# Kernel tuning notes

Measured on AMD Instinct MI355X. Metric: run time of the kernel, lower is better.

## Reference

```python
import jax, jax.numpy as jnp
import numpy as np

NUM_NODES = 50000
NODE_DIM = 32
EDGE_DIM = 7
HIDDEN_DIM = 64
NUM_EDGES = 200000


def setup_inputs() -> dict:
    key = jax.random.key(0)
    ks = jax.random.split(key, 12)
    s = lambda *d: 1.0 / np.sqrt(d[0])
    return {
        "edge_index": jax.random.randint(ks[0], (2, NUM_EDGES), 0, NUM_NODES, dtype=jnp.int64)
        if jax.config.jax_enable_x64 else jax.random.randint(ks[0], (2, NUM_EDGES), 0, NUM_NODES, dtype=jnp.int32),
        "edge_attr": jax.random.normal(ks[1], (NUM_EDGES, EDGE_DIM), dtype=jnp.float32),
        # learned parameters
        "node_emb": jax.random.normal(ks[2], (NUM_NODES, NODE_DIM), dtype=jnp.float32),
        "w_nn": jax.random.normal(ks[3], (EDGE_DIM, NODE_DIM * HIDDEN_DIM), dtype=jnp.float32) * s(EDGE_DIM),
        "b_nn": jnp.zeros((NODE_DIM * HIDDEN_DIM,), dtype=jnp.float32),
        "root_w": jax.random.normal(ks[4], (NODE_DIM, HIDDEN_DIM), dtype=jnp.float32) * s(NODE_DIM),
        "conv_bias": jnp.zeros((HIDDEN_DIM,), dtype=jnp.float32),
        "w_e1": jax.random.normal(ks[5], (2 * HIDDEN_DIM + EDGE_DIM, 64), dtype=jnp.float32) * s(2 * HIDDEN_DIM + EDGE_DIM),
        "b_e1": jnp.zeros((64,), dtype=jnp.float32),
        "w_e2": jax.random.normal(ks[6], (64, 2), dtype=jnp.float32) * s(64),
        "b_e2": jnp.zeros((2,), dtype=jnp.float32),
    }


def reference(edge_index, edge_attr, node_emb, w_nn, b_nn, root_w, conv_bias,
              w_e1, b_e1, w_e2, b_e2):
    src, dst = edge_index[0], edge_index[1]
    x = node_emb  # [N, node_dim]
    # NNConv: per-edge weight matrix from edge MLP (Linear + ReLU)
    w_edge = jax.nn.relu(edge_attr @ w_nn + b_nn).reshape(-1, NODE_DIM, HIDDEN_DIM)  # [E, in, out]
    # gather source features, per-edge matmul, scatter-add to dst (aggr='add')
    msg = jnp.einsum("ei,eio->eo", x[src], w_edge)  # [E, hidden]
    agg = jax.ops.segment_sum(msg, dst, num_segments=NUM_NODES)  # [N, hidden]
    h = jax.nn.relu(agg + x @ root_w + conv_bias)  # conv root term + bias, then outer ReLU
    # edge classifier MLP
    edge_repr = jnp.concatenate([h[src], h[dst], edge_attr], axis=1)  # [E, 2H+edge_dim]
    out = jax.nn.relu(edge_repr @ w_e1 + b_e1) @ w_e2 + b_e2  # [E, 2]
    return out
```

## Files before the change

### kernel.cpp

```cpp
#include <hip/hip_runtime.h>
#include <hip/hip_bf16.h>

#define NUM_NODES 50000
#define NODE_DIM 32
#define EDGE_DIM 7
#define HIDDEN_DIM 64
#define NUM_EDGES 200000

#define INIT_BLOCKS ((NUM_NODES + 127) / 128)
#define PREP_BLOCKS ((5 * 4 * 64 * 8 + 255) / 256)

typedef __attribute__((ext_vector_type(8))) short bf16x8;
typedef __attribute__((ext_vector_type(4))) float f32x4;
typedef _Float16 h2v __attribute__((ext_vector_type(2)));

__device__ inline unsigned f2bf(float f) {
    union { float f; unsigned u; } x; x.f = f;
    return (x.u + 0x7FFFu + ((x.u >> 16) & 1u)) >> 16;
}
__device__ inline unsigned pack2bf(float a, float b) {
    return f2bf(a) | (f2bf(b) << 16);
}
__device__ inline h2v u2h(unsigned u) {
    union { unsigned u; h2v h; } c; c.u = u; return c.h;
}
__device__ inline unsigned h2u(h2v h) {
    union { h2v h; unsigned u; } c; c.h = h; return c.u;
}
__device__ inline unsigned packh2(float a, float b) {
    h2v h; h[0] = (_Float16)a; h[1] = (_Float16)b; return h2u(h);
}

__global__ __launch_bounds__(256) void k_initprep(const float* __restrict__ x,
                                                  const float* __restrict__ root_w,
                                                  const float* __restrict__ conv_bias,
                                                  const float* __restrict__ w_e1,
                                                  const float* __restrict__ b_e1,
                                                  float* __restrict__ agg,
                                                  ushort* __restrict__ bfrag) {
    if (blockIdx.x >= INIT_BLOCKS) {
        int u = (blockIdx.x - INIT_BLOCKS) * blockDim.x + threadIdx.x;
        if (u < 5 * 4 * 64 * 8) {
            int j     = u & 7;
            int lane  = (u >> 3) & 63;
            int ntile = (u >> 9) & 3;
            int kstep = u >> 11;
            int k = kstep * 32 + (lane >> 4) * 8 + j;
            int o = ntile * 16 + (lane & 15);
            float v = (k < 135) ? w_e1[k * 64 + o] : ((k == 135) ? b_e1[o] : 0.f);
            bfrag[u] = (ushort)f2bf(v);
        }
        return;
    }
    __shared__ float rw[NODE_DIM * HIDDEN_DIM];
    __shared__ float cb[HIDDEN_DIM];
    __shared__ float xS[128 * NODE_DIM];
    for (int t = threadIdx.x; t < NODE_DIM * HIDDEN_DIM; t += 256) rw[t] = root_w[t];
    if (threadIdx.x < HIDDEN_DIM) cb[threadIdx.x] = conv_bias[threadIdx.x];
    const int nb = blockIdx.x * 128;
    {
        const float4* xg = (const float4*)x;
        float4* xs4 = (float4*)xS;
        #pragma unroll
        for (int r = 0; r < 4; ++r) {
            int t = r * 256 + threadIdx.x;
            int gi = nb * (NODE_DIM / 4) + t;
            xs4[t] = (gi < NUM_NODES * (NODE_DIM / 4)) ? xg[gi] : make_float4(0.f, 0.f, 0.f, 0.f);
        }
    }
    __syncthreads();
    const int lane = threadIdx.x & 63;
    const int w    = threadIdx.x >> 6;
    for (int r = 0; r < 32; ++r) {
        const int n = nb + w * 32 + r;
        if (n >= NUM_NODES) break;
        float acc = cb[lane];
        const float* xr = &xS[(w * 32 + r) * NODE_DIM];
        #pragma unroll
        for (int i = 0; i < NODE_DIM; ++i)
            acc = fmaf(xr[i], rw[i * HIDDEN_DIM + lane], acc);
        agg[n * HIDDEN_DIM + lane] = acc;
    }
}

#define MBX 8
__global__ __launch_bounds__(512) void k_msg10(const int* __restrict__ ei,
                                               const float* __restrict__ ea,
                                               const float* __restrict__ x,
                                               const float* __restrict__ w_nn,
                                               const float* __restrict__ b_nn,
                                               float* __restrict__ agg) {
    __shared__ uint4    wAu[16 * 64];
    __shared__ uint4    wBu[16 * 64];
    __shared__ unsigned xHu[8][MBX][16];
    __shared__ float    eS[8][MBX][8];
    for (int c = threadIdx.x; c < 16 * 64; c += 512) {
        const int p = c >> 6, o = c & 63;
        const int c0 = (2 * p) * 64 + o, c1 = c0 + 64;
        uint4 a, b;
        a.x = packh2(w_nn[c0],            w_nn[c1]);
        a.y = packh2(w_nn[2048 + c0],     w_nn[2048 + c1]);
        a.z = packh2(w_nn[2 * 2048 + c0], w_nn[2 * 2048 + c1]);
        a.w = packh2(w_nn[3 * 2048 + c0], w_nn[3 * 2048 + c1]);
        b.x = packh2(w_nn[4 * 2048 + c0], w_nn[4 * 2048 + c1]);
        b.y = packh2(w_nn[5 * 2048 + c0], w_nn[5 * 2048 + c1]);
        b.z = packh2(w_nn[6 * 2048 + c0], w_nn[6 * 2048 + c1]);
        b.w = packh2(b_nn[c0],            b_nn[c1]);
        wAu[c] = a; wBu[c] = b;
    }
    __syncthreads();

    const int lane   = threadIdx.x & 63;
    const int ws     = threadIdx.x >> 6;
    const int wave   = (blockIdx.x * blockDim.x + threadIdx.x) >> 6;
    const int nwaves = (gridDim.x * blockDim.x) >> 6;

    for (int e0 = wave * MBX; e0 < NUM_EDGES; e0 += nwaves * MBX) {
        int sD[MBX];
        #pragma unroll
        for (int m = 0; m < MBX; ++m)
            sD[m] = __builtin_amdgcn_readfirstlane(ei[NUM_EDGES + e0 + m]);

        {
            const int m  = lane >> 3;
            const int q4 = lane & 7;
            const int s  = ei[e0 + m];
            const float4 xv = *(const float4*)(x + (size_t)s * NODE_DIM + q4 * 4);
            xHu[ws][m][2 * q4 + 0] = packh2(xv.x, xv.y);
            xHu[ws][m][2 * q4 + 1] = packh2(xv.z, xv.w);
            if (lane < MBX * EDGE_DIM)
                eS[ws][lane / EDGE_DIM][lane % EDGE_DIM] = ea[(size_t)e0 * EDGE_DIM + lane];
        }

        float acc[MBX];
        #pragma unroll
        for (int m = 0; m < MBX; ++m) acc[m] = 0.f;

        #pragma unroll
        for (int half = 0; half < 2; ++half) {
            h2v evR[4][7];
            #pragma unroll
            for (int j = 0; j < 4; ++j) {
                const float4* e4 = (const float4*)&eS[ws][half * 4 + j][0];
                const float4 a0 = e4[0], a1 = e4[1];
                evR[j][0] = (h2v)((_Float16)a0.x);
                evR[j][1] = (h2v)((_Float16)a0.y);
                evR[j][2] = (h2v)((_Float16)a0.z);
                evR[j][3] = (h2v)((_Float16)a0.w);
                evR[j][4] = (h2v)((_Float16)a1.x);
                evR[j][5] = (h2v)((_Float16)a1.y);
                evR[j][6] = (h2v)((_Float16)a1.z);
            }

            #pragma unroll 2
            for (int p4 = 0; p4 < 4; ++p4) {
                uint4 xr[4];
                #pragma unroll
                for (int j = 0; j < 4; ++j)
                    xr[j] = *(const uint4*)&xHu[ws][half * 4 + j][p4 * 4];
                #pragma unroll
                for (int pp = 0; pp < 4; ++pp) {
                    const int p = p4 * 4 + pp;
                    const uint4 wa = wAu[p * 64 + lane];
                    const uint4 wb = wBu[p * 64 + lane];
                    #pragma unroll
                    for (int j = 0; j < 4; ++j) {
                        h2v t = u2h(wb.w);
                        t = evR[j][0] * u2h(wa.x) + t;
                        t = evR[j][1] * u2h(wa.y) + t;
                        t = evR[j][2] * u2h(wa.z) + t;
                        t = evR[j][3] * u2h(wa.w) + t;
                        t = evR[j][4] * u2h(wb.x) + t;
                        t = evR[j][5] * u2h(wb.y) + t;
                        t = evR[j][6] * u2h(wb.z) + t;
                        t = __builtin_elementwise_max(t, (h2v)((_Float16)0.f));
                        const unsigned xp = (pp == 0) ? xr[j].x : (pp == 1) ? xr[j].y
                                          : (pp == 2) ? xr[j].z : xr[j].w;
                        acc[half * 4 + j] = __builtin_amdgcn_fdot2(
                            t, u2h(xp), acc[half * 4 + j], false);
                    }
                }
            }
        }

        #pragma unroll
        for (int m = 0; m < MBX; ++m)
            atomicAdd(&agg[(size_t)sD[m] * HIDDEN_DIM + lane], acc[m]);
    }
}

#define ASTRIDE 168
__global__ __launch_bounds__(256) void k_edge3(const int* __restrict__ ei,
                                               const float* __restrict__ ea,
                                               const float* __restrict__ agg,
                                               const ushort* __restrict__ bfrag,
                                               const float* __restrict__ w_e2,
                                               const float* __restrict__ b_e2,
                                               float* __restrict__ out) {
    __shared__ ushort aS[64 * ASTRIDE];
    __shared__ ushort bS[5 * 4 * 64 * 8];
    __shared__ float  w2S[128];
    {
        const uint4* g = (const uint4*)bfrag;
        uint4* s = (uint4*)bS;
        for (int t = threadIdx.x; t < 1280; t += 256) s[t] = g[t];
        if (threadIdx.x < 128) w2S[threadIdx.x] = w_e2[threadIdx.x];
    }
    const int e0 = blockIdx.x * 64;
    {
        const int el = threadIdx.x >> 2;
        const int q  = threadIdx.x & 3;
        const int e  = e0 + el;
        const int src = ei[e], dst = ei[NUM_EDGES + e];
        const float4* ps = (const float4*)(agg + (size_t)src * HIDDEN_DIM + q * 16);
        const float4* pd = (const float4*)(agg + (size_t)dst * HIDDEN_DIM + q * 16);
        unsigned* arow = (unsigned*)(aS + el * ASTRIDE);
        #pragma unroll
        for (int i = 0; i < 4; ++i) {
            float4 s = ps[i];
            arow[q * 8 + i * 2 + 0] = pack2bf(fmaxf(s.x, 0.f), fmaxf(s.y, 0.f));
            arow[q * 8 + i * 2 + 1] = pack2bf(fmaxf(s.z, 0.f), fmaxf(s.w, 0.f));
        }
        #pragma unroll
        for (int i = 0; i < 4; ++i) {
            float4 d = pd[i];
            arow[32 + q * 8 + i * 2 + 0] = pack2bf(fmaxf(d.x, 0.f), fmaxf(d.y, 0.f));
            arow[32 + q * 8 + i * 2 + 1] = pack2bf(fmaxf(d.z, 0.f), fmaxf(d.w, 0.f));
        }
        if (q == 0) {
            float ev[8];
            #pragma unroll
            for (int k = 0; k < EDGE_DIM; ++k) ev[k] = ea[e * EDGE_DIM + k];
            ev[7] = 1.0f;
            #pragma unroll
            for (int i = 0; i < 4; ++i)
                arow[64 + i] = pack2bf(ev[2 * i], ev[2 * i + 1]);
        } else {
            unsigned* z = arow + 64 + q * 4;
            z[0] = 0u; z[1] = 0u; z[2] = 0u; z[3] = 0u;
        }
    }
    __syncthreads();

    const int lane = threadIdx.x & 63;
    const int w    = threadIdx.x >> 6;
    f32x4 acc[4];
    #pragma unroll
    for (int nt = 0; nt < 4; ++nt) acc[nt] = (f32x4){0.f, 0.f, 0.f, 0.f};

    const ushort* arow = aS + (w * 16 + (lane & 15)) * ASTRIDE + (lane >> 4) * 8;
    #pragma unroll
    for (int ks = 0; ks < 5; ++ks) {
        bf16x8 af = *(const bf16x8*)(arow + ks * 32);
        #pragma unroll
        for (int nt = 0; nt < 4; ++nt) {
            bf16x8 bf = *(const bf16x8*)(bS + ((ks * 4 + nt) * 64 + lane) * 8);
            acc[nt] = __builtin_amdgcn_mfma_f32_16x16x32_bf16(af, bf, acc[nt], 0, 0, 0);
        }
    }

    float w20[4], w21[4];
    #pragma unroll
    for (int nt = 0; nt < 4; ++nt) {
        int o = nt * 16 + (lane & 15);
        w20[nt] = w2S[o * 2 + 0];
        w21[nt] = w2S[o * 2 + 1];
    }
    const float bias0 = b_e2[0], bias1 = b_e2[1];
    #pragma unroll
    for (int r = 0; r < 4; ++r) {
        float p0 = 0.f, p1 = 0.f;
        #pragma unroll
        for (int nt = 0; nt < 4; ++nt) {
            float z = fmaxf(acc[nt][r], 0.f);
            p0 = fmaf(z, w20[nt], p0);
            p1 = fmaf(z, w21[nt], p1);
        }
        #pragma unroll
        for (int off = 1; off < 16; off <<= 1) {
            p0 += __shfl_xor(p0, off);
            p1 += __shfl_xor(p1, off);
        }
        if ((lane & 15) == 0) {
            int e = e0 + w * 16 + (lane >> 4) * 4 + r;
            float2 v; v.x = p0 + bias0; v.y = p1 + bias1;
            ((float2*)out)[e] = v;
        }
    }
}

extern "C" void kernel_launch(void* const* d_in, const int* in_sizes, int n_in,
                              void* d_out, int out_size, void* d_ws, size_t ws_size,
                              hipStream_t stream) {
    const int*   ei        = (const int*)d_in[0];
    const float* edge_attr = (const float*)d_in[1];
    const float* node_emb  = (const float*)d_in[2];
    const float* w_nn      = (const float*)d_in[3];
    const float* b_nn      = (const float*)d_in[4];
    const float* root_w    = (const float*)d_in[5];
    const float* conv_bias = (const float*)d_in[6];
    const float* w_e1      = (const float*)d_in[7];
    const float* b_e1      = (const float*)d_in[8];
    const float* w_e2      = (const float*)d_in[9];
    const float* b_e2      = (const float*)d_in[10];
    float*       out       = (float*)d_out;
    float*       agg       = (float*)d_ws;
    ushort*      bfrag     = (ushort*)((char*)d_ws + 12800000);

    k_initprep<<<INIT_BLOCKS + PREP_BLOCKS, 256, 0, stream>>>(
        node_emb, root_w, conv_bias, w_e1, b_e1, agg, bfrag);
    k_msg10<<<1024, 512, 0, stream>>>(ei, edge_attr, node_emb, w_nn, b_nn, agg);
    k_edge3<<<NUM_EDGES / 64, 256, 0, stream>>>(ei, edge_attr, agg, bfrag, w_e2, b_e2, out);
}
```

Measured before the change: 120.3 us.

## Store node aggregation buffer in fp16 with packed fp16 atomic adds

The node aggregation buffer changes from fp32 to fp16 across all three kernels. The init kernel writes packed half pairs. The message kernel scatters with global_atomic_pk_add_f16, so it issues half as many atomics. The edge kernel gathers half as many bytes per node. This cuts atomic traffic and gather bandwidth, but it risks accuracy loss and overflow from accumulating sums in fp16.

```diff
diff --git a/kernel.cpp b/kernel.cpp
--- a/kernel.cpp
+++ b/kernel.cpp
@@ -36,7 +36,7 @@
                                                   const float* __restrict__ conv_bias,
                                                   const float* __restrict__ w_e1,
                                                   const float* __restrict__ b_e1,
-                                                  float* __restrict__ agg,
+                                                  ushort* __restrict__ aggh,
                                                   ushort* __restrict__ bfrag) {
     if (blockIdx.x >= INIT_BLOCKS) {
         int u = (blockIdx.x - INIT_BLOCKS) * blockDim.x + threadIdx.x;
@@ -79,17 +79,19 @@
         #pragma unroll
         for (int i = 0; i < NODE_DIM; ++i)
             acc = fmaf(xr[i], rw[i * HIDDEN_DIM + lane], acc);
-        agg[n * HIDDEN_DIM + lane] = acc;
+        const float nbr = __shfl_down(acc, 1);
+        if (!(lane & 1))
+            ((unsigned*)(aggh + (size_t)n * HIDDEN_DIM))[lane >> 1] = packh2(acc, nbr);
     }
 }
 
 #define MBX 8
-__global__ __launch_bounds__(512) void k_msg10(const int* __restrict__ ei,
+__global__ __launch_bounds__(512) void k_msg12(const int* __restrict__ ei,
                                                const float* __restrict__ ea,
                                                const float* __restrict__ x,
                                                const float* __restrict__ w_nn,
                                                const float* __restrict__ b_nn,
-                                               float* __restrict__ agg) {
+                                               ushort* __restrict__ aggh) {
     __shared__ uint4    wAu[16 * 64];
     __shared__ uint4    wBu[16 * 64];
     __shared__ unsigned xHu[8][MBX][16];
@@ -184,15 +186,22 @@
         }
 
         #pragma unroll
-        for (int m = 0; m < MBX; ++m)
-            atomicAdd(&agg[(size_t)sD[m] * HIDDEN_DIM + lane], acc[m]);
+        for (int m = 0; m < MBX; ++m) {
+            const float nbr = __shfl_down(acc[m], 1);
+            if (!(lane & 1)) {
+                const unsigned pk = packh2(acc[m], nbr);
+                ushort* ap = aggh + (size_t)sD[m] * HIDDEN_DIM + lane;
+                asm volatile("global_atomic_pk_add_f16 %0, %1, off"
+                             :: "v"(ap), "v"(pk) : "memory");
+            }
+        }
     }
 }
 
 #define ASTRIDE 168
 __global__ __launch_bounds__(256) void k_edge3(const int* __restrict__ ei,
                                                const float* __restrict__ ea,
-                                               const float* __restrict__ agg,
+                                               const ushort* __restrict__ aggh,
                                                const ushort* __restrict__ bfrag,
                                                const float* __restrict__ w_e2,
                                                const float* __restrict__ b_e2,
@@ -212,20 +221,30 @@
         const int q  = threadIdx.x & 3;
         const int e  = e0 + el;
         const int src = ei[e], dst = ei[NUM_EDGES + e];
-        const float4* ps = (const float4*)(agg + (size_t)src * HIDDEN_DIM + q * 16);
-        const float4* pd = (const float4*)(agg + (size_t)dst * HIDDEN_DIM + q * 16);
+        const uint4* ps = (const uint4*)(aggh + (size_t)src * HIDDEN_DIM + q * 16);
+        const uint4* pd = (const uint4*)(aggh + (size_t)dst * HIDDEN_DIM + q * 16);
         unsigned* arow = (unsigned*)(aS + el * ASTRIDE);
         #pragma unroll
-        for (int i = 0; i < 4; ++i) {
-            float4 s = ps[i];
-            arow[q * 8 + i * 2 + 0] = pack2bf(fmaxf(s.x, 0.f), fmaxf(s.y, 0.f));
-            arow[q * 8 + i * 2 + 1] = pack2bf(fmaxf(s.z, 0.f), fmaxf(s.w, 0.f));
-        }
-        #pragma unroll
-        for (int i = 0; i < 4; ++i) {
-            float4 d = pd[i];
-            arow[32 + q * 8 + i * 2 + 0] = pack2bf(fmaxf(d.x, 0.f), fmaxf(d.y, 0.f));
-            arow[32 + q * 8 + i * 2 + 1] = pack2bf(fmaxf(d.z, 0.f), fmaxf(d.w, 0.f));
+        for (int i = 0; i < 2; ++i) {
+            const uint4 sv = ps[i];
+            const unsigned uu[4] = {sv.x, sv.y, sv.z, sv.w};
+            #pragma unroll
+            for (int jj = 0; jj < 4; ++jj) {
+                h2v hh = u2h(uu[jj]);
+                arow[q * 8 + i * 4 + jj] =
+                    pack2bf(fmaxf((float)hh[0], 0.f), fmaxf((float)hh[1], 0.f));
+            }
+        }
+        #pragma unroll
+        for (int i = 0; i < 2; ++i) {
+            const uint4 dv = pd[i];
+            const unsigned uu[4] = {dv.x, dv.y, dv.z, dv.w};
+            #pragma unroll
+            for (int jj = 0; jj < 4; ++jj) {
+                h2v hh = u2h(uu[jj]);
+                arow[32 + q * 8 + i * 4 + jj] =
+                    pack2bf(fmaxf((float)hh[0], 0.f), fmaxf((float)hh[1], 0.f));
+            }
         }
         if (q == 0) {
             float ev[8];
@@ -304,11 +323,11 @@
     const float* w_e2      = (const float*)d_in[9];
     const float* b_e2      = (const float*)d_in[10];
     float*       out       = (float*)d_out;
-    float*       agg       = (float*)d_ws;
+    ushort*      aggh      = (ushort*)d_ws;
     ushort*      bfrag     = (ushort*)((char*)d_ws + 12800000);
 
     k_initprep<<<INIT_BLOCKS + PREP_BLOCKS, 256, 0, stream>>>(
-        node_emb, root_w, conv_bias, w_e1, b_e1, agg, bfrag);
-    k_msg10<<<1024, 512, 0, stream>>>(ei, edge_attr, node_emb, w_nn, b_nn, agg);
-    k_edge3<<<NUM_EDGES / 64, 256, 0, stream>>>(ei, edge_attr, agg, bfrag, w_e2, b_e2, out);
-}
+        node_emb, root_w, conv_bias, w_e1, b_e1, aggh, bfrag);
+    k_msg12<<<1024, 512, 0, stream>>>(ei, edge_attr, node_emb, w_nn, b_nn, aggh);
+    k_edge3<<<NUM_EDGES / 64, 256, 0, stream>>>(ei, edge_attr, aggh, bfrag, w_e2, b_e2, out);
+}
```

New measurement: 118.5 us (median of 2 runs). No clear change (-1.5%).
